# Kernel tuning notes

Hardware: AMD Instinct MI355X
Metric: run time of the kernel (lower is better)

## Reference

```python
import jax, jax.numpy as jnp
import numpy as np

B, L, D_MODEL, H, D_K, D_V = 64, 52, 4096, 32, 128, 128
NEW_C = D_MODEL // H  # per-head input channel after the (faithful) raw reshape


def setup_inputs() -> dict:
    key = jax.random.key(0)
    ks = jax.random.split(key, 12)
    s = 0.02
    return {
        "Q": jax.random.normal(ks[0], (B, L, D_MODEL), jnp.float32),
        "K": jax.random.normal(ks[1], (B, L, D_MODEL), jnp.float32),
        "V": jax.random.normal(ks[2], (B, L, D_MODEL), jnp.float32),
        "Wq": jax.random.normal(ks[3], (H, NEW_C, D_K), jnp.float32) * s,
        "bq": jnp.zeros((H, D_K), jnp.float32),
        "Wk": jax.random.normal(ks[4], (H, NEW_C, D_K), jnp.float32) * s,
        "bk": jnp.zeros((H, D_K), jnp.float32),
        "Wv": jax.random.normal(ks[5], (H, NEW_C, D_V), jnp.float32) * s,
        "bv": jnp.zeros((H, D_V), jnp.float32),
        "Wo": jax.random.normal(ks[6], (H * D_V, D_MODEL), jnp.float32) * s,
        "bo": jnp.zeros((D_MODEL,), jnp.float32),
    }


def reference(Q, K, V, Wq, bq, Wk, bk, Wv, bv, Wo, bo):
    # Faithful to source: raw reshape (B, L, D) -> (B, H, L, D/H), NOT a channel split.
    def split(x):
        return x.reshape(B, H, L, NEW_C)

    q = jnp.einsum('bhlc,hck->bhlk', split(Q), Wq) + bq[None, :, None, :]  # (B,H,L,D_K)
    k = jnp.einsum('bhlc,hck->bhlk', split(K), Wk) + bk[None, :, None, :]
    v = jnp.einsum('bhlc,hcv->bhlv', split(V), Wv) + bv[None, :, None, :]

    scores = jnp.einsum('bhqk,bhmk->bhqm', q, k) / jnp.sqrt(jnp.asarray(D_K, q.dtype))
    # causal mask: keep j <= i, else -inf (matches the numpy masking loop)
    causal = jnp.tril(jnp.ones((L, L), bool))
    scores = jnp.where(causal[None, None], scores, -jnp.inf)
    attn = jax.nn.softmax(scores, axis=-1)
    o = jnp.einsum('bhqm,bhmv->bhqv', attn, v)  # (B,H,L,D_V)
    o = o.transpose(0, 2, 1, 3).reshape(B, L, H * D_V)  # concat heads on last axis
    # Dropout(0.1) is identity at inference.
    return o @ Wo + bo
```

## Files before the change

### kernel.cpp

```cpp
#include <hip/hip_runtime.h>
#include <hip/hip_bf16.h>

#define B_SZ   64
#define L_SZ   52
#define DMODEL 4096
#define H_SZ   32
#define C_SZ   128
#define DK     128

#define GM 3328
#define GN 4096
#define GK 4096

typedef __bf16 bf16x8 __attribute__((ext_vector_type(8)));
typedef float  f32x4  __attribute__((ext_vector_type(4)));

__device__ __forceinline__ void gload_lds16(const void* g, void* l) {
  __builtin_amdgcn_global_load_lds(
      (__attribute__((address_space(1))) void*)(void*)g,
      (__attribute__((address_space(3))) void*)l, 16, 0, 0);
}

__global__ __launch_bounds__(256) void wo_transpose_kernel(
    const float* __restrict__ Wo, __hip_bfloat16* __restrict__ WoT) {
  __shared__ float tile[64][65];
  const int nt = blockIdx.x, mt = blockIdx.y;
  const int t = threadIdx.x;
  const int r  = t >> 4;
  const int c4 = (t & 15) << 2;
#pragma unroll
  for (int p = 0; p < 4; ++p) {
    const int rr = r + p * 16;
    const float4 v = *(const float4*)(Wo + (size_t)(mt * 64 + rr) * 4096 + nt * 64 + c4);
    tile[rr][c4 + 0] = v.x; tile[rr][c4 + 1] = v.y;
    tile[rr][c4 + 2] = v.z; tile[rr][c4 + 3] = v.w;
  }
  __syncthreads();
#pragma unroll
  for (int p = 0; p < 4; ++p) {
    const int rr = r + p * 16;
    union { __hip_bfloat16 h[4]; ushort4 u; } o4;
#pragma unroll
    for (int e = 0; e < 4; ++e) o4.h[e] = __float2bfloat16(tile[c4 + e][rr]);
    *(ushort4*)(WoT + (size_t)(nt * 64 + rr) * 4096 + mt * 64 + c4) = o4.u;
  }
}

__global__ __launch_bounds__(256) void w3_transpose_kernel(
    const float* __restrict__ Wq, const float* __restrict__ Wk,
    const float* __restrict__ Wv, __hip_bfloat16* __restrict__ WqT,
    __hip_bfloat16* __restrict__ WkT, __hip_bfloat16* __restrict__ WvT) {
  __shared__ float tile[64][65];
  const int bz = blockIdx.z;
  const float* in = (bz < 32 ? Wq : (bz < 64 ? Wk : Wv)) + (size_t)(bz & 31) * 16384;
  __hip_bfloat16* out = (bz < 32 ? WqT : (bz < 64 ? WkT : WvT)) + (size_t)(bz & 31) * 16384;
  const int nt = blockIdx.x, mt = blockIdx.y;
  const int t = threadIdx.x;
  const int r  = t >> 4;
  const int c4 = (t & 15) << 2;
#pragma unroll
  for (int p = 0; p < 4; ++p) {
    const int rr = r + p * 16;
    const float4 v = *(const float4*)(in + (size_t)(mt * 64 + rr) * 128 + nt * 64 + c4);
    tile[rr][c4 + 0] = v.x; tile[rr][c4 + 1] = v.y;
    tile[rr][c4 + 2] = v.z; tile[rr][c4 + 3] = v.w;
  }
  __syncthreads();
#pragma unroll
  for (int p = 0; p < 4; ++p) {
    const int rr = r + p * 16;
    union { __hip_bfloat16 h[4]; ushort4 u; } o4;
#pragma unroll
    for (int e = 0; e < 4; ++e) o4.h[e] = __float2bfloat16(tile[c4 + e][rr]);
    *(ushort4*)(out + (size_t)(nt * 64 + rr) * 128 + mt * 64 + c4) = o4.u;
  }
}

template <bool TRANSPOSED>
__device__ __forceinline__ void wave_proj(
    const __hip_bfloat16* __restrict__ xs, const __hip_bfloat16* __restrict__ WT,
    const float* __restrict__ bias, __hip_bfloat16* __restrict__ out,
    int n0, int r16, int kq) {
  f32x4 acc[4][2] = {};
  bf16x8 bfrag[2][4];
#pragma unroll
  for (int nt = 0; nt < 2; ++nt)
#pragma unroll
    for (int kk = 0; kk < 4; ++kk)
      bfrag[nt][kk] = *(const bf16x8*)(WT + (n0 + nt * 16 + r16) * 128 + kk * 32 + kq * 8);
#pragma unroll
  for (int kk = 0; kk < 4; ++kk) {
    bf16x8 a[4];
#pragma unroll
    for (int mt = 0; mt < 4; ++mt)
      a[mt] = *(const bf16x8*)(xs + (mt * 16 + r16) * 136 + kk * 32 + kq * 8);
#pragma unroll
    for (int mt = 0; mt < 4; ++mt)
#pragma unroll
      for (int nt = 0; nt < 2; ++nt)
        acc[mt][nt] = __builtin_amdgcn_mfma_f32_16x16x32_bf16(a[mt], bfrag[nt][kk], acc[mt][nt], 0, 0, 0);
  }
#pragma unroll
  for (int nt = 0; nt < 2; ++nt) {
    const int col = n0 + nt * 16 + r16;
    const float bv = bias[col];
#pragma unroll
    for (int mt = 0; mt < 4; ++mt) {
      const int m0 = mt * 16 + kq * 4;
      if (!TRANSPOSED) {
#pragma unroll
        for (int i = 0; i < 4; ++i)
          out[(m0 + i) * 136 + col] = __float2bfloat16(acc[mt][nt][i] + bv);
      } else {
        union { __hip_bfloat16 h[4]; ushort4 u; } o4;
        if (m0 < 52) {
#pragma unroll
          for (int i = 0; i < 4; ++i) o4.h[i] = __float2bfloat16(acc[mt][nt][i] + bv);
        } else {
          o4.u = make_ushort4(0, 0, 0, 0);
        }
        *(ushort4*)(out + col * 72 + m0) = o4.u;
      }
    }
  }
}

__global__ __launch_bounds__(256, 2) void attn_kernel(
    const float* __restrict__ Qin, const float* __restrict__ Kin,
    const float* __restrict__ Vin,
    const __hip_bfloat16* __restrict__ WqT, const float* __restrict__ bq,
    const __hip_bfloat16* __restrict__ WkT, const float* __restrict__ bk,
    const __hip_bfloat16* __restrict__ WvT, const float* __restrict__ bv,
    __hip_bfloat16* __restrict__ Oc) {
  __shared__ __align__(16) char lds[70656];
  __hip_bfloat16* xs0  = (__hip_bfloat16*)(lds);
  __hip_bfloat16* xs1  = (__hip_bfloat16*)(lds + 17408);
  __hip_bfloat16* xs2  = (__hip_bfloat16*)(lds + 34816);
  __hip_bfloat16* vT   = (__hip_bfloat16*)(lds + 52224);
  __hip_bfloat16* q_sh = (__hip_bfloat16*)(lds + 34816);
  __hip_bfloat16* k_sh = (__hip_bfloat16*)(lds);
  float*          s_sh = (float*)(lds + 17408);
  __hip_bfloat16* p_sh = (__hip_bfloat16*)(lds + 34816);

  const int h = blockIdx.x, bb = blockIdx.y;
  const int t = threadIdx.x;
  const int w = t >> 6, lane = t & 63;
  const int r16 = lane & 15, kq = lane >> 4;
  const size_t xoff = (size_t)bb * (L_SZ * DMODEL) + (size_t)h * (L_SZ * C_SZ);

  {
    const float* xp[3] = {Qin + xoff, Kin + xoff, Vin + xoff};
    __hip_bfloat16* xd[3] = {xs0, xs1, xs2};
#pragma unroll
    for (int tz = 0; tz < 3; ++tz) {
      const float* X = xp[tz];
      __hip_bfloat16* xs = xd[tz];
      for (int idx = t; idx < 52 * 32; idx += 256) {
        const int row = idx >> 5, c4 = (idx & 31) << 2;
        const float4 v = *(const float4*)(X + row * 128 + c4);
        union { __hip_bfloat16 h[4]; ushort4 u; } o4;
        o4.h[0] = __float2bfloat16(v.x); o4.h[1] = __float2bfloat16(v.y);
        o4.h[2] = __float2bfloat16(v.z); o4.h[3] = __float2bfloat16(v.w);
        *(ushort4*)(xs + row * 136 + c4) = o4.u;
      }
      if (t < 12 * 17) {
        const int row = 52 + t / 17, c8 = (t % 17) * 8;
        *(uint4*)(xs + row * 136 + c8) = make_uint4(0, 0, 0, 0);
      }
    }
  }
  __syncthreads();

  wave_proj<true>(xs2, WvT + (size_t)h * 16384, bv + h * 128, vT, w * 32, r16, kq);
  __syncthreads();
  wave_proj<false>(xs0, WqT + (size_t)h * 16384, bq + h * 128, q_sh, w * 32, r16, kq);
  __syncthreads();
  wave_proj<false>(xs1, WkT + (size_t)h * 16384, bk + h * 128, k_sh, w * 32, r16, kq);
  __syncthreads();

  {
    const int n0 = w * 16;
    f32x4 sacc[4] = {};
#pragma unroll
    for (int kk = 0; kk < 4; ++kk) {
      const bf16x8 bf_ = *(const bf16x8*)(k_sh + (n0 + r16) * 136 + kk * 32 + kq * 8);
#pragma unroll
      for (int mt = 0; mt < 4; ++mt) {
        const bf16x8 a = *(const bf16x8*)(q_sh + (mt * 16 + r16) * 136 + kk * 32 + kq * 8);
        sacc[mt] = __builtin_amdgcn_mfma_f32_16x16x32_bf16(a, bf_, sacc[mt], 0, 0, 0);
      }
    }
    const float scale = 0.08838834764831845f;
#pragma unroll
    for (int mt = 0; mt < 4; ++mt)
#pragma unroll
      for (int i = 0; i < 4; ++i)
        s_sh[(mt * 16 + kq * 4 + i) * 68 + n0 + r16] = sacc[mt][i] * scale;
  }
  __syncthreads();

  {
    const int r = t >> 2, qd = t & 3;
    if (r < 52) {
      float v[16];
      float mx = -3e38f;
#pragma unroll
      for (int j4 = 0; j4 < 4; ++j4) {
        const f32x4 s4 = *(const f32x4*)(s_sh + r * 68 + qd * 16 + j4 * 4);
#pragma unroll
        for (int e = 0; e < 4; ++e) {
          const int col = qd * 16 + j4 * 4 + e;
          const float val = (col <= r) ? s4[e] : -3e38f;
          v[j4 * 4 + e] = val;
          mx = fmaxf(mx, val);
        }
      }
      mx = fmaxf(mx, __shfl_xor(mx, 1));
      mx = fmaxf(mx, __shfl_xor(mx, 2));
      float ex[16];
      float sum = 0.f;
#pragma unroll
      for (int j = 0; j < 16; ++j) {
        const int col = qd * 16 + j;
        const float e = (col <= r) ? __expf(v[j] - mx) : 0.f;
        ex[j] = e; sum += e;
      }
      sum += __shfl_xor(sum, 1);
      sum += __shfl_xor(sum, 2);
      const float inv = 1.0f / sum;
      union { __hip_bfloat16 h[8]; uint4 q; } p0, p1;
#pragma unroll
      for (int j = 0; j < 8; ++j) {
        p0.h[j] = __float2bfloat16(ex[j] * inv);
        p1.h[j] = __float2bfloat16(ex[8 + j] * inv);
      }
      *(uint4*)(p_sh + r * 72 + qd * 16)     = p0.q;
      *(uint4*)(p_sh + r * 72 + qd * 16 + 8) = p1.q;
    } else {
      *(uint4*)(p_sh + r * 72 + qd * 16)     = make_uint4(0, 0, 0, 0);
      *(uint4*)(p_sh + r * 72 + qd * 16 + 8) = make_uint4(0, 0, 0, 0);
    }
  }
  __syncthreads();

  {
    const int n0 = w * 32;
    f32x4 oacc[4][2] = {};
#pragma unroll
    for (int kk = 0; kk < 2; ++kk) {
      bf16x8 bfr[2];
#pragma unroll
      for (int nt = 0; nt < 2; ++nt)
        bfr[nt] = *(const bf16x8*)(vT + (n0 + nt * 16 + r16) * 72 + kk * 32 + kq * 8);
#pragma unroll
      for (int mt = 0; mt < 4; ++mt) {
        const bf16x8 a = *(const bf16x8*)(p_sh + (mt * 16 + r16) * 72 + kk * 32 + kq * 8);
#pragma unroll
        for (int nt = 0; nt < 2; ++nt)
          oacc[mt][nt] = __builtin_amdgcn_mfma_f32_16x16x32_bf16(a, bfr[nt], oacc[mt][nt], 0, 0, 0);
      }
    }
    const size_t obase = (size_t)bb * 52 * 4096 + (size_t)h * 128;
#pragma unroll
    for (int nt = 0; nt < 2; ++nt) {
      const int col = n0 + nt * 16 + r16;
#pragma unroll
      for (int mt = 0; mt < 4; ++mt) {
        const int row0 = mt * 16 + kq * 4;
#pragma unroll
        for (int i = 0; i < 4; ++i) {
          const int row = row0 + i;
          if (row < 52)
            Oc[obase + (size_t)row * 4096 + col] = __float2bfloat16(oacc[mt][nt][i]);
        }
      }
    }
  }
}

#define STAGE(GBASE, REGOFF, KT, KS, WB) do {                                  \
    const __hip_bfloat16* s_ = (GBASE) + (size_t)(KT) * 64 + (KS) * 32;        \
    char* d_ = (WB) + (REGOFF) + ((KS) ? 16384 : 0) + t * 16;                  \
    gload_lds16(s_, d_);                                                       \
    gload_lds16(s_ + (size_t)128 * GK, d_ + 8192);                             \
  } while (0)

#define PHASE(KS, MH, STAGE_STMT, EXTRA_WAIT)                                  \
  {                                                                            \
    bf16x8 af[4];                                                              \
    _Pragma("unroll")                                                          \
    for (int mf = 0; mf < 4; ++mf)                                             \
      af[mf] = *(const bf16x8*)(rb + (KS) * 16384 + aBase + ((MH) * 4 + mf) * 1024); \
    if ((MH) == 0) {                                                           \
      _Pragma("unroll")                                                        \
      for (int nf = 0; nf < 4; ++nf)                                           \
        bf[nf] = *(const bf16x8*)(rb + 32768 + (KS) * 16384 + bBase + nf * 1024); \
    }                                                                          \
    STAGE_STMT;                                                                \
    __builtin_amdgcn_s_barrier();                                              \
    asm volatile("s_waitcnt lgkmcnt(0)" ::: "memory");                         \
    __builtin_amdgcn_sched_barrier(0);                                         \
    __builtin_amdgcn_s_setprio(1);                                             \
    _Pragma("unroll")                                                          \
    for (int mf = 0; mf < 4; ++mf)                                             \
      _Pragma("unroll")                                                        \
      for (int nf = 0; nf < 4; ++nf)                                           \
        acc[(MH) * 4 + mf][nf] = __builtin_amdgcn_mfma_f32_16x16x32_bf16(      \
            af[mf], bf[nf], acc[(MH) * 4 + mf][nf], 0, 0, 0);                  \
    __builtin_amdgcn_s_setprio(0);                                             \
    EXTRA_WAIT;                                                                \
    __builtin_amdgcn_s_barrier();                                              \
  }

__global__ __launch_bounds__(512, 2) void out_gemm_kernel(
    const __hip_bfloat16* __restrict__ A, const __hip_bfloat16* __restrict__ Bt,
    const float* __restrict__ bias, float* __restrict__ C) {
  __shared__ __align__(16) char lds[131072];

  int bid = blockIdx.x;
  bid = (bid & 7) * 26 + (bid >> 3);
  const int tm = bid >> 4;
  const int tn = bid & 15;

  const int t = threadIdx.x;
  const int w = t >> 6, lane = t & 63;
  const int wm = w >> 2, wn = w & 3;
  const int r16 = lane & 15, kq = lane >> 4;

  const int srow = t >> 2;
  const int sgslot = (t & 3) ^ ((srow >> 1) & 3);
  const __hip_bfloat16* gA0 = A  + (size_t)(tm * 256 + srow) * GK + sgslot * 8;
  const __hip_bfloat16* gB0 = Bt + (size_t)(tn * 256 + srow) * GK + sgslot * 8;

  const int slotr = kq ^ ((r16 >> 1) & 3);
  const int aBase = (wm * 128 + r16) * 64 + slotr * 16;
  const int bBase = (wn * 64 + r16) * 64 + slotr * 16;

  f32x4 acc[8][4] = {};

  STAGE(gA0, 0,     0, 0, lds);
  STAGE(gB0, 32768, 0, 0, lds);
  STAGE(gA0, 0,     0, 1, lds);
  STAGE(gB0, 32768, 0, 1, lds);
  STAGE(gA0, 0,     1, 0, lds + 65536);
  STAGE(gB0, 32768, 1, 0, lds + 65536);
  asm volatile("s_waitcnt vmcnt(4)" ::: "memory");
  __builtin_amdgcn_s_barrier();

#pragma unroll 1
  for (int kt = 0; kt < 64; ++kt) {
    const char* rb = lds + ((kt & 1) << 16);
    char* wb1 = lds + (((kt + 1) & 1) << 16);
    char* wb2 = (char*)rb;
    const int st1 = kt + 1 < 64 ? kt + 1 : 63;
    const int st2 = kt + 2 < 64 ? kt + 2 : 63;
    bf16x8 bf[4];
    PHASE(0, 0, STAGE(gA0, 0,     st1, 1, wb1), )
    PHASE(0, 1, STAGE(gB0, 32768, st1, 1, wb1), )
    PHASE(1, 0, STAGE(gA0, 0,     st2, 0, wb2), )
    PHASE(1, 1, STAGE(gB0, 32768, st2, 0, wb2),
          asm volatile("s_waitcnt vmcnt(4)" ::: "memory"))
  }
  asm volatile("s_waitcnt vmcnt(0)" ::: "memory");

  const int row0 = tm * 256 + wm * 128 + kq * 4;
  const int col0 = tn * 256 + wn * 64 + r16;
#pragma unroll
  for (int nf = 0; nf < 4; ++nf) {
    const int col = col0 + nf * 16;
    const float bv = bias[col];
#pragma unroll
    for (int mf = 0; mf < 8; ++mf) {
      const int row = row0 + mf * 16;
#pragma unroll
      for (int i = 0; i < 4; ++i)
        C[(size_t)(row + i) * GN + col] = acc[mf][nf][i] + bv;
    }
  }
}

extern "C" void kernel_launch(void* const* d_in, const int* in_sizes, int n_in,
                              void* d_out, int out_size, void* d_ws, size_t ws_size,
                              hipStream_t stream) {
  const float* Q  = (const float*)d_in[0];
  const float* K  = (const float*)d_in[1];
  const float* V  = (const float*)d_in[2];
  const float* Wq = (const float*)d_in[3];
  const float* bq = (const float*)d_in[4];
  const float* Wk = (const float*)d_in[5];
  const float* bk = (const float*)d_in[6];
  const float* Wv = (const float*)d_in[7];
  const float* bv = (const float*)d_in[8];
  const float* Wo = (const float*)d_in[9];
  const float* bo = (const float*)d_in[10];
  float* out = (float*)d_out;

  char* wsb = (char*)d_ws;
  __hip_bfloat16* WoT = (__hip_bfloat16*)wsb;
  __hip_bfloat16* Oc  = (__hip_bfloat16*)(wsb + (size_t)GN * GK * 2);
  __hip_bfloat16* WqT = (__hip_bfloat16*)(wsb + (size_t)GN * GK * 2 + (size_t)GM * GN * 2);
  __hip_bfloat16* WkT = WqT + (size_t)H_SZ * C_SZ * DK;
  __hip_bfloat16* WvT = WkT + (size_t)H_SZ * C_SZ * DK;

  w3_transpose_kernel<<<dim3(2, 2, 96), 256, 0, stream>>>(Wq, Wk, Wv, WqT, WkT, WvT);
  wo_transpose_kernel<<<dim3(64, 64), 256, 0, stream>>>(Wo, WoT);
  attn_kernel<<<dim3(H_SZ, B_SZ), 256, 0, stream>>>(Q, K, V, WqT, bq, WkT, bk, WvT, bv, Oc);
  out_gemm_kernel<<<dim3(13 * 16), 512, 0, stream>>>(Oc, WoT, bo, out);
}
```

Before: 218.0 us.

## Software-pipeline LDS fragment loads with register double-buffering in output GEMM

Restructures the output-projection GEMM main loop so the A/B fragments for the next MFMA cluster are read from LDS into a second register set while the current cluster computes. Global-to-LDS staging is regrouped: all four stage loads for tile kt+2 are issued together after a single barrier, replacing the per-phase interleaving, so each k-tile needs two barriers instead of eight. The aim is to hide LDS read latency behind MFMAs and cut barrier overhead. It costs extra vector registers for the second fragment set, which under launch_bounds(512,2) could cause spills. The global loads for a whole tile are now bunched together rather than spread across phases.

New measurement: 230.9 us. +5.9%, slower.

```diff
diff --git a/kernel.cpp b/kernel.cpp
--- a/kernel.cpp
+++ b/kernel.cpp
@@ -285,32 +285,30 @@
     gload_lds16(s_ + (size_t)128 * GK, d_ + 8192);                             \
   } while (0)
 
-#define PHASE(KS, MH, STAGE_STMT, EXTRA_WAIT)                                  \
-  {                                                                            \
-    bf16x8 af[4];                                                              \
+#define WAIT_LGKM0()                                                           \
+  asm volatile("s_waitcnt lgkmcnt(0)" ::: "memory");                           \
+  __builtin_amdgcn_sched_barrier(0)
+
+#define LOAD_AF(DST, BASE)                                                     \
+  _Pragma("unroll")                                                            \
+  for (int mf = 0; mf < 4; ++mf)                                               \
+    DST[mf] = *(const bf16x8*)((BASE) + mf * 1024)
+
+#define LOAD_BF(DST, BASE)                                                     \
+  _Pragma("unroll")                                                            \
+  for (int nf = 0; nf < 4; ++nf)                                               \
+    DST[nf] = *(const bf16x8*)((BASE) + nf * 1024)
+
+#define CLUSTER(AF, BF, MQ)                                                    \
+  __builtin_amdgcn_sched_barrier(0);                                           \
+  __builtin_amdgcn_s_setprio(1);                                               \
+  _Pragma("unroll")                                                            \
+  for (int mf = 0; mf < 4; ++mf)                                               \
     _Pragma("unroll")                                                          \
-    for (int mf = 0; mf < 4; ++mf)                                             \
-      af[mf] = *(const bf16x8*)(rb + (KS) * 16384 + aBase + ((MH) * 4 + mf) * 1024); \
-    if ((MH) == 0) {                                                           \
-      _Pragma("unroll")                                                        \
-      for (int nf = 0; nf < 4; ++nf)                                           \
-        bf[nf] = *(const bf16x8*)(rb + 32768 + (KS) * 16384 + bBase + nf * 1024); \
-    }                                                                          \
-    STAGE_STMT;                                                                \
-    __builtin_amdgcn_s_barrier();                                              \
-    asm volatile("s_waitcnt lgkmcnt(0)" ::: "memory");                         \
-    __builtin_amdgcn_sched_barrier(0);                                         \
-    __builtin_amdgcn_s_setprio(1);                                             \
-    _Pragma("unroll")                                                          \
-    for (int mf = 0; mf < 4; ++mf)                                             \
-      _Pragma("unroll")                                                        \
-      for (int nf = 0; nf < 4; ++nf)                                           \
-        acc[(MH) * 4 + mf][nf] = __builtin_amdgcn_mfma_f32_16x16x32_bf16(      \
-            af[mf], bf[nf], acc[(MH) * 4 + mf][nf], 0, 0, 0);                  \
-    __builtin_amdgcn_s_setprio(0);                                             \
-    EXTRA_WAIT;                                                                \
-    __builtin_amdgcn_s_barrier();                                              \
-  }
+    for (int nf = 0; nf < 4; ++nf)                                             \
+      acc[(MQ) * 4 + mf][nf] = __builtin_amdgcn_mfma_f32_16x16x32_bf16(        \
+          AF[mf], BF[nf], acc[(MQ) * 4 + mf][nf], 0, 0, 0);                    \
+  __builtin_amdgcn_s_setprio(0)
 
 __global__ __launch_bounds__(512, 2) void out_gemm_kernel(
     const __hip_bfloat16* __restrict__ A, const __hip_bfloat16* __restrict__ Bt,
@@ -333,35 +331,59 @@
   const __hip_bfloat16* gB0 = Bt + (size_t)(tn * 256 + srow) * GK + sgslot * 8;
 
   const int slotr = kq ^ ((r16 >> 1) & 3);
-  const int aBase = (wm * 128 + r16) * 64 + slotr * 16;
-  const int bBase = (wn * 64 + r16) * 64 + slotr * 16;
+  const int aB0 = (wm * 128 + r16) * 64 + slotr * 16;
+  const int bB  = 32768 + (wn * 64 + r16) * 64 + slotr * 16;
 
   f32x4 acc[8][4] = {};
+  bf16x8 af0[4], af1[4], bf0[4], bf1[4];
 
   STAGE(gA0, 0,     0, 0, lds);
+  STAGE(gA0, 0,     0, 1, lds);
   STAGE(gB0, 32768, 0, 0, lds);
-  STAGE(gA0, 0,     0, 1, lds);
   STAGE(gB0, 32768, 0, 1, lds);
   STAGE(gA0, 0,     1, 0, lds + 65536);
+  STAGE(gA0, 0,     1, 1, lds + 65536);
   STAGE(gB0, 32768, 1, 0, lds + 65536);
-  asm volatile("s_waitcnt vmcnt(4)" ::: "memory");
+  STAGE(gB0, 32768, 1, 1, lds + 65536);
+  asm volatile("s_waitcnt vmcnt(8)" ::: "memory");
   __builtin_amdgcn_s_barrier();
+  LOAD_AF(af0, lds + aB0);
+  LOAD_BF(bf0, lds + bB);
 
 #pragma unroll 1
   for (int kt = 0; kt < 64; ++kt) {
-    const char* rb = lds + ((kt & 1) << 16);
-    char* wb1 = lds + (((kt + 1) & 1) << 16);
-    char* wb2 = (char*)rb;
-    const int st1 = kt + 1 < 64 ? kt + 1 : 63;
-    const int st2 = kt + 2 < 64 ? kt + 2 : 63;
-    bf16x8 bf[4];
-    PHASE(0, 0, STAGE(gA0, 0,     st1, 1, wb1), )
-    PHASE(0, 1, STAGE(gB0, 32768, st1, 1, wb1), )
-    PHASE(1, 0, STAGE(gA0, 0,     st2, 0, wb2), )
-    PHASE(1, 1, STAGE(gB0, 32768, st2, 0, wb2),
-          asm volatile("s_waitcnt vmcnt(4)" ::: "memory"))
-  }
-  asm volatile("s_waitcnt vmcnt(0)" ::: "memory");
+    char* rb = lds + ((kt & 1) << 16);
+    char* nb = lds + (((kt + 1) & 1) << 16);
+
+    WAIT_LGKM0();
+    LOAD_AF(af1, rb + 4096 + aB0);
+    CLUSTER(af0, bf0, 0);
+
+    WAIT_LGKM0();
+    LOAD_AF(af0, rb + 16384 + aB0);
+    LOAD_BF(bf1, rb + 16384 + bB);
+    CLUSTER(af1, bf0, 1);
+
+    WAIT_LGKM0();
+    LOAD_AF(af1, rb + 16384 + 4096 + aB0);
+    CLUSTER(af0, bf1, 0);
+
+    WAIT_LGKM0();
+    __builtin_amdgcn_s_barrier();
+    {
+      const int st2 = kt + 2 < 64 ? kt + 2 : 63;
+      STAGE(gA0, 0,     st2, 0, rb);
+      STAGE(gA0, 0,     st2, 1, rb);
+      STAGE(gB0, 32768, st2, 0, rb);
+      STAGE(gB0, 32768, st2, 1, rb);
+    }
+    asm volatile("s_waitcnt vmcnt(8)" ::: "memory");
+    __builtin_amdgcn_s_barrier();
+    LOAD_AF(af0, nb + aB0);
+    LOAD_BF(bf0, nb + bB);
+    CLUSTER(af1, bf1, 1);
+  }
+  asm volatile("s_waitcnt vmcnt(0) lgkmcnt(0)" ::: "memory");
 
   const int row0 = tm * 256 + wm * 128 + kq * 4;
   const int col0 = tn * 256 + wn * 64 + r16;
```
